# Performance work log

Measured on AMD Instinct MI355X. Metric: run time of the kernel, lower is better.

Reference implementation:

```python
import jax, jax.numpy as jnp
import numpy as np

B, S, D, H = 2, 2048, 1024, 16
DK = D // H
THETA = 10000.0


def _freqs_cos_sin(dim, seq_len, theta=THETA):
    # matches precompute_freqs_cis: freqs over full d_model, pairs of adjacent dims
    inv = 1.0 / theta ** (np.arange(0, dim, 2)[: dim // 2].astype(np.float32) / dim)
    t = np.arange(seq_len, dtype=np.float32)
    ang = np.outer(t, inv)  # [S, D/2]
    return jnp.asarray(np.cos(ang)), jnp.asarray(np.sin(ang))


def setup_inputs() -> dict:
    key = jax.random.key(0)
    ks = jax.random.split(key, 11)
    sc = 1.0 / np.sqrt(D)
    cos, sin = _freqs_cos_sin(D, S)
    return {
        "query": jax.random.normal(ks[0], (B, S, D), jnp.float32),
        "key": jax.random.normal(ks[1], (B, S, D), jnp.float32),
        "value": jax.random.normal(ks[2], (B, S, D), jnp.float32),
        "wq": jax.random.normal(ks[3], (D, D), jnp.float32) * sc,
        "bq": jnp.zeros((D,), jnp.float32),
        "wk": jax.random.normal(ks[4], (D, D), jnp.float32) * sc,
        "bk": jnp.zeros((D,), jnp.float32),
        "wv": jax.random.normal(ks[5], (D, D), jnp.float32) * sc,
        "bv": jnp.zeros((D,), jnp.float32),
        "wo": jax.random.normal(ks[6], (D, D), jnp.float32) * sc,
        "bo": jnp.zeros((D,), jnp.float32),
        "cos": cos,  # [S, D/2]
        "sin": sin,  # [S, D/2]
    }


def _rope(x, cos, sin):
    # x: [B,S,D]; pairs are adjacent elements along D (view_as_complex semantics)
    xr = x.reshape(*x.shape[:-1], -1, 2)  # [B,S,D/2,2]
    x0, x1 = xr[..., 0], xr[..., 1]
    c, s = cos[None], sin[None]  # broadcast over batch
    o0 = x0 * c - x1 * s
    o1 = x0 * s + x1 * c
    return jnp.stack([o0, o1], axis=-1).reshape(x.shape)


def reference(query, key, value, wq, bq, wk, bk, wv, bv, wo, bo, cos, sin):
    q = query @ wq.T + bq
    k = key @ wk.T + bk
    v = value @ wv.T + bv
    q = _rope(q, cos, sin)
    k = _rope(k, cos, sin)
    # split heads: [B,S,D] -> [B,H,S,DK]
    q = q.reshape(B, S, H, DK).transpose(0, 2, 1, 3)
    k = k.reshape(B, S, H, DK).transpose(0, 2, 1, 3)
    v = v.reshape(B, S, H, DK).transpose(0, 2, 1, 3)
    scores = jnp.einsum("bhqd,bhkd->bhqk", q, k) / jnp.sqrt(jnp.float32(DK))
    attn = jax.nn.softmax(scores, axis=-1)  # dropout is identity in eval
    out = jnp.einsum("bhqk,bhkd->bhqd", attn, v)
    out = out.transpose(0, 2, 1, 3).reshape(B, S, D)
    return out @ wo.T + bo
```

## Files before the change

kernel.cpp:

```cpp
#include <hip/hip_runtime.h>
#include <hip/hip_fp16.h>

typedef _Float16 f16;
using f16x8 = __attribute__((ext_vector_type(8))) _Float16;
using h2 = __attribute__((ext_vector_type(2))) __fp16;
using f32x4 = __attribute__((ext_vector_type(4))) float;
using f32x16 = __attribute__((ext_vector_type(16))) float;

#define LOG2E 1.4426950408889634f

__device__ __forceinline__ void gload16(const void* g, void* l) {
  __builtin_amdgcn_global_load_lds(
      (const __attribute__((address_space(1))) void*)g,
      (__attribute__((address_space(3))) void*)l, 16, 0, 0);
}

__device__ __forceinline__ float b32(h2 x) { return __builtin_bit_cast(float, x); }
__device__ __forceinline__ unsigned u32(h2 x) { return __builtin_bit_cast(unsigned, x); }

__global__ __launch_bounds__(256) void convert_k(
    const float* __restrict__ q, const float* __restrict__ k, const float* __restrict__ v,
    const float* __restrict__ wq, const float* __restrict__ wk,
    const float* __restrict__ wv, const float* __restrict__ wo,
    f16* __restrict__ dst) {
  const size_t SEG = (size_t)4 * 1024 * 1024;
  size_t i = ((size_t)blockIdx.x * 256 + threadIdx.x) * 8;
  const float* src; size_t off;
  if (i < SEG)            { src = q;  off = i; }
  else if (i < 2 * SEG)   { src = k;  off = i - SEG; }
  else if (i < 3 * SEG)   { src = v;  off = i - 2 * SEG; }
  else {
    size_t wi = i - 3 * SEG;
    int s = (int)(wi >> 20);
    src = (s == 0) ? wq : (s == 1) ? wk : (s == 2) ? wv : wo;
    off = wi & ((1u << 20) - 1);
  }
  float4 a = *(const float4*)(src + off);
  float4 b = *(const float4*)(src + off + 4);
  f16x8 o;
  o[0] = (f16)a.x; o[1] = (f16)a.y; o[2] = (f16)a.z; o[3] = (f16)a.w;
  o[4] = (f16)b.x; o[5] = (f16)b.y; o[6] = (f16)b.z; o[7] = (f16)b.w;
  *(f16x8*)(dst + i) = o;
}

template <int QKV>
__global__ __launch_bounds__(256) void gemm_k(
    const f16* __restrict__ Abase, const f16* __restrict__ Wbase,
    const float* __restrict__ b0, const float* __restrict__ b1, const float* __restrict__ b2,
    const float* __restrict__ cosT, const float* __restrict__ sinT,
    f16* __restrict__ qh, f16* __restrict__ kh, f16* __restrict__ vt,
    float* __restrict__ outF) {
  __shared__ f16 sm[4][128 * 32];
  int tid = threadIdx.x, wid = tid >> 6, lane = tid & 63;
  int z = QKV ? blockIdx.z : 0;
  const f16* A = Abase + (size_t)z * (4u * 1024 * 1024);
  const f16* W = Wbase + (size_t)z * (1024u * 1024);

  int lid = blockIdx.x + (blockIdx.y << 3);
  int xcd = lid & 7, q = lid >> 3;
  int m0 = (xcd * 4 + (q & 3)) * 128;
  int n0 = (q >> 2) * 128;
  int wr = wid >> 1, wc = wid & 1;
  f32x4 acc[4][4] = {};

  int srow = tid >> 2;
  int sslot = (tid & 3) ^ (srow & 3);
  const f16* asrc0 = A + (size_t)(m0 + srow) * 1024 + sslot * 8;
  const f16* asrc1 = A + (size_t)(m0 + 64 + srow) * 1024 + sslot * 8;
  const f16* bsrc0 = W + (size_t)(n0 + srow) * 1024 + sslot * 8;
  const f16* bsrc1 = W + (size_t)(n0 + 64 + srow) * 1024 + sslot * 8;

  int aoff[4], boff[4];
#pragma unroll
  for (int i = 0; i < 4; ++i) {
    int row = wr * 64 + i * 16 + (lane & 15);
    aoff[i] = row * 32 + (((lane >> 4) ^ (row & 3)) * 8);
    int col = wc * 64 + i * 16 + (lane & 15);
    boff[i] = col * 32 + (((lane >> 4) ^ (col & 3)) * 8);
  }

  gload16(asrc0, (void*)(&sm[0][0] + wid * 512));
  gload16(asrc1, (void*)(&sm[0][0] + 2048 + wid * 512));
  gload16(bsrc0, (void*)(&sm[2][0] + wid * 512));
  gload16(bsrc1, (void*)(&sm[2][0] + 2048 + wid * 512));

  int cur = 0;
  for (int kt = 0; kt < 32; ++kt) {
    if (kt < 31) {
      int k0 = (kt + 1) * 32;
      gload16(asrc0 + k0, (void*)(&sm[cur ^ 1][0] + wid * 512));
      gload16(asrc1 + k0, (void*)(&sm[cur ^ 1][0] + 2048 + wid * 512));
      gload16(bsrc0 + k0, (void*)(&sm[2 + (cur ^ 1)][0] + wid * 512));
      gload16(bsrc1 + k0, (void*)(&sm[2 + (cur ^ 1)][0] + 2048 + wid * 512));
      asm volatile("s_waitcnt vmcnt(4)" ::: "memory");
    } else {
      asm volatile("s_waitcnt vmcnt(0)" ::: "memory");
    }
    __builtin_amdgcn_s_barrier();
    __builtin_amdgcn_sched_barrier(0);
    f16x8 af[4], bf[4];
#pragma unroll
    for (int i = 0; i < 4; ++i) {
      af[i] = *(const f16x8*)(&sm[cur][0] + aoff[i]);
      bf[i] = *(const f16x8*)(&sm[2 + cur][0] + boff[i]);
    }
#pragma unroll
    for (int i = 0; i < 4; ++i)
#pragma unroll
      for (int j = 0; j < 4; ++j)
        acc[i][j] = __builtin_amdgcn_mfma_f32_16x16x32_f16(af[i], bf[j], acc[i][j], 0, 0, 0);
    __builtin_amdgcn_s_barrier();
    cur ^= 1;
  }

  const float* bias = QKV ? (z == 0 ? b0 : (z == 1 ? b1 : b2)) : b0;

  if (QKV) {
    f16* Ct = &sm[0][0];
#pragma unroll
    for (int i = 0; i < 4; ++i) {
#pragma unroll
      for (int j = 0; j < 4; ++j) {
#pragma unroll
        for (int r = 0; r < 4; ++r) {
          int row_l = wr * 64 + i * 16 + ((lane >> 4) << 2) + r;
          int col_l = wc * 64 + j * 16 + (lane & 15);
          int gcol = n0 + col_l;
          float val = acc[i][j][r] + bias[gcol];
          if (z < 2) {
            int s = (m0 + row_l) & 2047;
            float pr = __shfl_xor(val, 1);
            int j2 = gcol >> 1;
            float c = cosT[s * 512 + j2], sn = sinT[s * 512 + j2];
            val = (lane & 1) ? (c * val + sn * pr) : (c * val - sn * pr);
            if (z == 0) val *= 0.125f * LOG2E;
          }
          Ct[row_l * 128 + (col_l ^ ((row_l & 7) << 3))] = (f16)val;
        }
      }
    }
    __syncthreads();
    int bb = m0 >> 11, sbase = m0 & 2047;
    if (z < 2) {
      int row = tid >> 1, halfsel = tid & 1;
      int h = (n0 >> 6) + halfsel;
      f16* dst = (z == 0 ? qh : kh) +
                 (((size_t)bb * 16 + h) * 2048 + sbase + row) * 64;
#pragma unroll
      for (int ch = 0; ch < 8; ++ch) {
        int c = halfsel * 64 + ch * 8;
        f16x8 v = *(const f16x8*)(Ct + row * 128 + (c ^ ((row & 7) << 3)));
        *(f16x8*)(dst + ch * 8) = v;
      }
    } else {
      int c = tid & 127, halfsel = tid >> 7;
      int h = (n0 >> 6) + (c >> 6), dk = c & 63;
      f16* dst = vt + (((size_t)bb * 16 + h) * 64 + dk) * 2048 + sbase + halfsel * 64;
#pragma unroll
      for (int g = 0; g < 8; ++g) {
        f16x8 v;
#pragma unroll
        for (int e = 0; e < 8; ++e) {
          int r = halfsel * 64 + g * 8 + e;
          v[e] = Ct[r * 128 + (c ^ ((r & 7) << 3))];
        }
        *(f16x8*)(dst + g * 8) = v;
      }
    }
  } else {
#pragma unroll
    for (int i = 0; i < 4; ++i) {
#pragma unroll
      for (int j = 0; j < 4; ++j) {
#pragma unroll
        for (int r = 0; r < 4; ++r) {
          int grow = m0 + wr * 64 + i * 16 + ((lane >> 4) << 2) + r;
          int gcol = n0 + wc * 64 + j * 16 + (lane & 15);
          outF[(size_t)grow * 1024 + gcol] = acc[i][j][r] + bias[gcol];
        }
      }
    }
  }
}

__global__ __launch_bounds__(256, 4) void flash_k(
    const f16* __restrict__ qh, const f16* __restrict__ kh, const f16* __restrict__ vt,
    f16* __restrict__ op, float2* __restrict__ mlbuf) {
  __shared__ f16 Ks[2][64 * 64];
  __shared__ f16 Vs[2][64 * 64];
  int tid = threadIdx.x, wid = tid >> 6, lane = tid & 63;
  int l31 = lane & 31, hi = lane >> 5;
  int qt = blockIdx.x, h = blockIdx.y, z = blockIdx.z;
  int b = z >> 1, ks = z & 1;
  size_t bh = (size_t)b * 16 + h;
  const f16* qp = qh + bh * (2048 * 64);
  const f16* kp = kh + bh * (2048 * 64) + (size_t)ks * 1024 * 64;
  const f16* vp = vt + bh * (64 * 2048) + ks * 1024;
  int qrow = qt * 128 + wid * 32 + l31;

  f16x8 qf[4];
#pragma unroll
  for (int kk = 0; kk < 4; ++kk)
    qf[kk] = *(const f16x8*)(qp + (size_t)qrow * 64 + kk * 16 + hi * 8);

  int srowA = tid >> 3, srowB = srowA + 32;
  int schA = (tid & 7) ^ (srowA & 7);
  int schB = (tid & 7) ^ (srowB & 7);
  const f16* ksrcA = kp + (size_t)srowA * 64 + schA * 8;
  const f16* ksrcB = kp + (size_t)srowB * 64 + schB * 8;
  const f16* vsrcA = vp + (size_t)srowA * 2048 + schA * 8;
  const f16* vsrcB = vp + (size_t)srowB * 2048 + schB * 8;

  int offr[2][4];
#pragma unroll
  for (int kb = 0; kb < 2; ++kb)
#pragma unroll
    for (int kk = 0; kk < 4; ++kk) {
      int row = kb * 32 + l31;
      offr[kb][kk] = (row * 128 + kk * 32 + hi * 16) ^ ((row & 7) << 4);
    }

  float m_ = -1e30f, l_ = 0.f;
  f32x16 oacc[2] = {};

  gload16(ksrcA, (char*)&Ks[0][0] + tid * 16);
  gload16(ksrcB, (char*)&Ks[0][0] + 4096 + tid * 16);
  gload16(vsrcA, (char*)&Vs[0][0] + tid * 16);
  gload16(vsrcB, (char*)&Vs[0][0] + 4096 + tid * 16);

  int cur = 0;
  for (int kt = 0; kt < 16; ++kt) {
    if (kt < 15) {
      gload16(ksrcA + (size_t)(kt + 1) * 4096, (char*)&Ks[cur ^ 1][0] + tid * 16);
      gload16(ksrcB + (size_t)(kt + 1) * 4096, (char*)&Ks[cur ^ 1][0] + 4096 + tid * 16);
      gload16(vsrcA + (size_t)(kt + 1) * 64, (char*)&Vs[cur ^ 1][0] + tid * 16);
      gload16(vsrcB + (size_t)(kt + 1) * 64, (char*)&Vs[cur ^ 1][0] + 4096 + tid * 16);
      asm volatile("s_waitcnt vmcnt(4)" ::: "memory");
    } else {
      asm volatile("s_waitcnt vmcnt(0)" ::: "memory");
    }
    __builtin_amdgcn_s_barrier();
    __builtin_amdgcn_sched_barrier(0);

    const char* kbase = (const char*)&Ks[cur][0];
    f32x16 sacc[2] = {};
#pragma unroll
    for (int kb = 0; kb < 2; ++kb)
#pragma unroll
      for (int kk = 0; kk < 4; ++kk) {
        f16x8 af = *(const f16x8*)(kbase + offr[kb][kk]);
        sacc[kb] = __builtin_amdgcn_mfma_f32_32x32x16_f16(af, qf[kk], sacc[kb], 0, 0, 0);
      }

    float t16[16];
#pragma unroll
    for (int i = 0; i < 16; ++i) t16[i] = fmaxf(sacc[0][i], sacc[1][i]);
#pragma unroll
    for (int s = 8; s; s >>= 1)
#pragma unroll
      for (int i = 0; i < s; ++i) t16[i] = fmaxf(t16[i], t16[i + s]);
    float pmax = fmaxf(t16[0], __shfl_xor(t16[0], 32));

    if (!__all(pmax <= m_ + 8.0f)) {
      float mn = fmaxf(m_, pmax);
      float al = __builtin_amdgcn_exp2f(m_ - mn);
      m_ = mn;
      l_ *= al;
#pragma unroll
      for (int mb = 0; mb < 2; ++mb)
#pragma unroll
        for (int i = 0; i < 16; ++i) oacc[mb][i] *= al;
    }

#pragma unroll
    for (int kb = 0; kb < 2; ++kb)
#pragma unroll
      for (int i = 0; i < 16; ++i)
        sacc[kb][i] = __builtin_amdgcn_exp2f(sacc[kb][i] - m_);
#pragma unroll
    for (int i = 0; i < 16; ++i) t16[i] = sacc[0][i] + sacc[1][i];
#pragma unroll
    for (int s = 8; s; s >>= 1)
#pragma unroll
      for (int i = 0; i < s; ++i) t16[i] += t16[i + s];
    l_ += t16[0] + __shfl_xor(t16[0], 32);

    f16x8 pa[4];
#pragma unroll
    for (int kk = 0; kk < 4; ++kk) {
      int kb = kk >> 1, c8 = (kk & 1) * 8;
      float wA = b32(__builtin_amdgcn_cvt_pkrtz(sacc[kb][c8 + 0], sacc[kb][c8 + 1]));
      float wB = b32(__builtin_amdgcn_cvt_pkrtz(sacc[kb][c8 + 2], sacc[kb][c8 + 3]));
      float wC = b32(__builtin_amdgcn_cvt_pkrtz(sacc[kb][c8 + 4], sacc[kb][c8 + 5]));
      float wD = b32(__builtin_amdgcn_cvt_pkrtz(sacc[kb][c8 + 6], sacc[kb][c8 + 7]));
      float oA = __shfl_xor(wA, 32), oB = __shfl_xor(wB, 32);
      float oC = __shfl_xor(wC, 32), oD = __shfl_xor(wD, 32);
      float4 ff;
      ff.x = hi ? oC : wA;
      ff.y = hi ? oD : wB;
      ff.z = hi ? wC : oA;
      ff.w = hi ? wD : oB;
      pa[kk] = __builtin_bit_cast(f16x8, ff);
    }

    const char* vbase = (const char*)&Vs[cur][0];
#pragma unroll
    for (int kk = 0; kk < 4; ++kk)
#pragma unroll
      for (int mb = 0; mb < 2; ++mb) {
        f16x8 av = *(const f16x8*)(vbase + offr[mb][kk]);
        oacc[mb] = __builtin_amdgcn_mfma_f32_32x32x16_f16(av, pa[kk], oacc[mb], 0, 0, 0);
      }

    __builtin_amdgcn_s_barrier();
    cur ^= 1;
  }

  float inv = 1.f / l_;
  f16* orow = op + (((size_t)z * 16 + h) * 2048 + qrow) * 64;
#pragma unroll
  for (int mb = 0; mb < 2; ++mb)
#pragma unroll
    for (int g = 0; g < 4; ++g) {
      uint2 st;
      st.x = u32(__builtin_amdgcn_cvt_pkrtz(oacc[mb][4 * g + 0] * inv, oacc[mb][4 * g + 1] * inv));
      st.y = u32(__builtin_amdgcn_cvt_pkrtz(oacc[mb][4 * g + 2] * inv, oacc[mb][4 * g + 3] * inv));
      *(uint2*)(orow + mb * 32 + g * 8 + hi * 4) = st;
    }
  if (hi == 0)
    mlbuf[((size_t)z * 16 + h) * 2048 + qrow] = make_float2(m_, l_);
}

__global__ __launch_bounds__(256) void combine_k(
    const f16* __restrict__ op, const float2* __restrict__ ml, f16* __restrict__ attnout) {
  int t = blockIdx.x * 256 + threadIdx.x;
  int row = t >> 3, c8 = t & 7;
  int b = row >> 15, h = (row >> 11) & 15, qrow = row & 2047;
  size_t i0 = ((size_t)(b * 2 + 0) * 16 + h) * 2048 + qrow;
  size_t i1 = ((size_t)(b * 2 + 1) * 16 + h) * 2048 + qrow;
  float2 a = ml[i0], c = ml[i1];
  float M = fmaxf(a.x, c.x);
  float w1 = a.y * __builtin_amdgcn_exp2f(a.x - M);
  float w2 = c.y * __builtin_amdgcn_exp2f(c.x - M);
  float inv = 1.f / (w1 + w2);
  w1 *= inv; w2 *= inv;
  f16x8 o1 = *(const f16x8*)(op + i0 * 64 + c8 * 8);
  f16x8 o2 = *(const f16x8*)(op + i1 * 64 + c8 * 8);
  f16x8 o;
#pragma unroll
  for (int e = 0; e < 8; ++e)
    o[e] = (f16)(w1 * (float)o1[e] + w2 * (float)o2[e]);
  *(f16x8*)(attnout + ((size_t)b * 2048 + qrow) * 1024 + h * 64 + c8 * 8) = o;
}

extern "C" void kernel_launch(void* const* d_in, const int* in_sizes, int n_in,
                              void* d_out, int out_size, void* d_ws, size_t ws_size,
                              hipStream_t stream) {
  (void)in_sizes; (void)n_in; (void)out_size; (void)ws_size;
  const float* query = (const float*)d_in[0];
  const float* key   = (const float*)d_in[1];
  const float* value = (const float*)d_in[2];
  const float* wq = (const float*)d_in[3];
  const float* bq = (const float*)d_in[4];
  const float* wk = (const float*)d_in[5];
  const float* bk = (const float*)d_in[6];
  const float* wv = (const float*)d_in[7];
  const float* bv = (const float*)d_in[8];
  const float* wo = (const float*)d_in[9];
  const float* bo = (const float*)d_in[10];
  const float* cosT = (const float*)d_in[11];
  const float* sinT = (const float*)d_in[12];
  float* out = (float*)d_out;
  f16* ws = (f16*)d_ws;
  const size_t SEG = (size_t)4 * 1024 * 1024;
  f16* Xh = ws;
  f16* Wh = ws + 3 * SEG;
  f16* qh = ws + 16u * 1024 * 1024;
  f16* kh = qh + SEG;
  f16* vt = kh + SEG;
  f16* attnout = ws;
  f16* op = ws + SEG;
  float2* mlb = (float2*)(ws + 12u * 1024 * 1024);

  convert_k<<<8192, 256, 0, stream>>>(query, key, value, wq, wk, wv, wo, ws);
  gemm_k<1><<<dim3(8, 32, 3), 256, 0, stream>>>(Xh, Wh, bq, bk, bv, cosT, sinT,
                                                qh, kh, vt, nullptr);
  flash_k<<<dim3(16, 16, 4), 256, 0, stream>>>(qh, kh, vt, op, mlb);
  combine_k<<<2048, 256, 0, stream>>>(op, mlb, attnout);
  gemm_k<0><<<dim3(8, 32, 1), 256, 0, stream>>>(attnout, Wh + 3u * 1024 * 1024, bo,
                                                nullptr, nullptr, nullptr, nullptr,
                                                nullptr, nullptr, nullptr, out);
}
```

Measured before the change: 155.1 us.

## Triple-buffer GEMM K-loop and remap flash blocks to share heads per XCD

Measured after the change: 144.8 us. 1.07x faster.

```diff
diff --git a/kernel.cpp b/kernel.cpp
--- a/kernel.cpp
+++ b/kernel.cpp
@@ -50,7 +50,7 @@
     const float* __restrict__ cosT, const float* __restrict__ sinT,
     f16* __restrict__ qh, f16* __restrict__ kh, f16* __restrict__ vt,
     float* __restrict__ outF) {
-  __shared__ f16 sm[4][128 * 32];
+  __shared__ f16 sm[6][128 * 32];
   int tid = threadIdx.x, wid = tid >> 6, lane = tid & 63;
   int z = QKV ? blockIdx.z : 0;
   const f16* A = Abase + (size_t)z * (4u * 1024 * 1024);
@@ -79,19 +79,24 @@
     boff[i] = col * 32 + (((lane >> 4) ^ (col & 3)) * 8);
   }
 
-  gload16(asrc0, (void*)(&sm[0][0] + wid * 512));
-  gload16(asrc1, (void*)(&sm[0][0] + 2048 + wid * 512));
-  gload16(bsrc0, (void*)(&sm[2][0] + wid * 512));
-  gload16(bsrc1, (void*)(&sm[2][0] + 2048 + wid * 512));
-
-  int cur = 0;
+#define GSTAGE(KT, BUF)                                                        \
+  do {                                                                         \
+    int k0_ = (KT) * 32;                                                       \
+    gload16(asrc0 + k0_, (void*)(&sm[BUF][0] + wid * 512));                    \
+    gload16(asrc1 + k0_, (void*)(&sm[BUF][0] + 2048 + wid * 512));             \
+    gload16(bsrc0 + k0_, (void*)(&sm[3 + (BUF)][0] + wid * 512));              \
+    gload16(bsrc1 + k0_, (void*)(&sm[3 + (BUF)][0] + 2048 + wid * 512));       \
+  } while (0)
+
+  GSTAGE(0, 0);
+  GSTAGE(1, 1);
+
   for (int kt = 0; kt < 32; ++kt) {
-    if (kt < 31) {
-      int k0 = (kt + 1) * 32;
-      gload16(asrc0 + k0, (void*)(&sm[cur ^ 1][0] + wid * 512));
-      gload16(asrc1 + k0, (void*)(&sm[cur ^ 1][0] + 2048 + wid * 512));
-      gload16(bsrc0 + k0, (void*)(&sm[2 + (cur ^ 1)][0] + wid * 512));
-      gload16(bsrc1 + k0, (void*)(&sm[2 + (cur ^ 1)][0] + 2048 + wid * 512));
+    int cb = kt % 3;
+    if (kt + 2 < 32) {
+      GSTAGE(kt + 2, (kt + 2) % 3);
+      asm volatile("s_waitcnt vmcnt(8)" ::: "memory");
+    } else if (kt + 1 < 32) {
       asm volatile("s_waitcnt vmcnt(4)" ::: "memory");
     } else {
       asm volatile("s_waitcnt vmcnt(0)" ::: "memory");
@@ -101,8 +106,8 @@
     f16x8 af[4], bf[4];
 #pragma unroll
     for (int i = 0; i < 4; ++i) {
-      af[i] = *(const f16x8*)(&sm[cur][0] + aoff[i]);
-      bf[i] = *(const f16x8*)(&sm[2 + cur][0] + boff[i]);
+      af[i] = *(const f16x8*)(&sm[cb][0] + aoff[i]);
+      bf[i] = *(const f16x8*)(&sm[3 + cb][0] + boff[i]);
     }
 #pragma unroll
     for (int i = 0; i < 4; ++i)
@@ -110,8 +115,8 @@
       for (int j = 0; j < 4; ++j)
         acc[i][j] = __builtin_amdgcn_mfma_f32_16x16x32_f16(af[i], bf[j], acc[i][j], 0, 0, 0);
     __builtin_amdgcn_s_barrier();
-    cur ^= 1;
   }
+#undef GSTAGE
 
   const float* bias = QKV ? (z == 0 ? b0 : (z == 1 ? b1 : b2)) : b0;
 
@@ -190,7 +195,11 @@
   __shared__ f16 Vs[2][64 * 64];
   int tid = threadIdx.x, wid = tid >> 6, lane = tid & 63;
   int l31 = lane & 31, hi = lane >> 5;
-  int qt = blockIdx.x, h = blockIdx.y, z = blockIdx.z;
+  int bid = blockIdx.x;
+  int xcd = bid & 7, t = bid >> 3;
+  int qt = t & 15, phi = t >> 4;
+  int p = phi * 8 + xcd;
+  int h = p & 15, z = p >> 4;
   int b = z >> 1, ks = z & 1;
   size_t bh = (size_t)b * 16 + h;
   const f16* qp = qh + bh * (2048 * 64);
@@ -385,7 +394,7 @@
   convert_k<<<8192, 256, 0, stream>>>(query, key, value, wq, wk, wv, wo, ws);
   gemm_k<1><<<dim3(8, 32, 3), 256, 0, stream>>>(Xh, Wh, bq, bk, bv, cosT, sinT,
                                                 qh, kh, vt, nullptr);
-  flash_k<<<dim3(16, 16, 4), 256, 0, stream>>>(qh, kh, vt, op, mlb);
+  flash_k<<<1024, 256, 0, stream>>>(qh, kh, vt, op, mlb);
   combine_k<<<2048, 256, 0, stream>>>(op, mlb, attnout);
   gemm_k<0><<<dim3(8, 32, 1), 256, 0, stream>>>(attnout, Wh + 3u * 1024 * 1024, bo,
                                                 nullptr, nullptr, nullptr, nullptr,
```
